# Performance work log

Measured on AMD Instinct MI355X. Metric: run time of the kernel, lower is better.

Reference implementation:

```python
import jax, jax.numpy as jnp
import numpy as np

B, T, NH, NB = 16, 400, 100, 65
SR, BLOCK = 16000, 160
REV_LEN = SR  # Reverb(sampling_rate, sampling_rate)


def _fft_convolve(signal, kernel):
    # torch: pad signal right by n, kernel left by its length, multiply spectra, keep 2nd half
    n = signal.shape[-1]
    s = jnp.pad(signal, [(0, 0)] * (signal.ndim - 1) + [(0, n)])
    k = jnp.pad(kernel, [(0, 0)] * (kernel.ndim - 1) + [(kernel.shape[-1], 0)])
    out = jnp.fft.irfft(jnp.fft.rfft(s) * jnp.fft.rfft(k), s.shape[-1])
    return out[..., out.shape[-1] // 2:]


def _amp_to_impulse_response(amp, target_size):
    # amp: [..., n_bands] real magnitudes treated as zero-phase rfft coefficients
    ir = jnp.fft.irfft(jax.lax.complex(amp, jnp.zeros_like(amp)))  # [..., 2*(NB-1)]
    fs = ir.shape[-1]
    ir = jnp.roll(ir, fs // 2, axis=-1)
    win = 0.5 - 0.5 * jnp.cos(2.0 * np.pi * jnp.arange(fs, dtype=ir.dtype) / fs)  # periodic hann
    ir = ir * win
    ir = jnp.pad(ir, [(0, 0)] * (ir.ndim - 1) + [(0, target_size - fs)])
    return jnp.roll(ir, -fs // 2, axis=-1)


def setup_inputs() -> dict:
    key = jax.random.key(0)
    ks = jax.random.split(key, 6)
    pitch = 40.0 + 400.0 * jax.random.uniform(ks[0], (B, T, 1), dtype=jnp.float32)
    total_amp = jax.random.uniform(ks[1], (B, T), dtype=jnp.float32)
    harmo_amps = jax.random.uniform(ks[2], (B, NH, T), dtype=jnp.float32) + 1e-3
    noise_filter = 0.1 * jax.random.uniform(ks[3], (B, T, NB), dtype=jnp.float32)
    noise = 2.0 * jax.random.uniform(ks[4], (B, T, BLOCK), dtype=jnp.float32) - 1.0
    reverb_noise = 2.0 * jax.random.uniform(ks[5], (REV_LEN, 1), dtype=jnp.float32) - 1.0
    decay = jnp.asarray(5.0, jnp.float32)
    wet = jnp.asarray(0.0, jnp.float32)
    return dict(pitch=pitch, total_amp=total_amp, harmo_amps=harmo_amps,
                noise_filter=noise_filter, noise=noise, reverb_noise=reverb_noise,
                decay=decay, wet=wet, sampling_rate=SR, block_size=BLOCK)


def reference(pitch, total_amp, harmo_amps, noise_filter, noise, reverb_noise,
              decay, wet, sampling_rate, block_size):
    dt = pitch.dtype
    n_harm = harmo_amps.shape[1]
    harm_idx = jnp.arange(1, n_harm + 1, dtype=dt)
    # remove_above_nyquist: mask harmonics whose freq >= sr/2 (tiny epsilon kept, as in DDSP)
    freqs = pitch[:, :, 0][:, None, :] * harm_idx[None, :, None]          # [B,NH,T]
    aa = (freqs < (sampling_rate / 2)).astype(dt) + 1e-4
    amps = harmo_amps * aa
    amps = jnp.transpose(amps, (0, 2, 1))                                  # [B,T,NH]
    amps = amps / jnp.sum(amps, axis=-1, keepdims=True)
    amps = amps * total_amp[..., None]
    # nearest-neighbor upsample by block_size (F.interpolate default mode)
    amps_up = jnp.repeat(amps, block_size, axis=1)                         # [B,N,NH]
    pitch_up = jnp.repeat(pitch, block_size, axis=1)                       # [B,N,1]
    # harmonic additive synthesis
    omega = jnp.cumsum(2.0 * np.pi * pitch_up / sampling_rate, axis=1)     # [B,N,1]
    harmonic = jnp.sum(jnp.sin(omega * harm_idx) * amps_up, axis=-1, keepdims=True)
    # filtered noise branch
    impulse = _amp_to_impulse_response(noise_filter, block_size)           # [B,T,BLOCK]
    noise_f = _fft_convolve(noise, impulse)                                # [B,T,BLOCK]
    noise_f = noise_f.reshape(noise_f.shape[0], -1, 1)                     # [B,N,1]
    signal = harmonic + noise_f
    # reverb (forward with reverb=True)
    rev_len = reverb_noise.shape[0]
    t = (jnp.arange(rev_len, dtype=dt) / sampling_rate)[None, :, None]     # [1,L,1]
    imp = reverb_noise[None] * jnp.exp(-jax.nn.softplus(-decay) * t * 500.0) * jax.nn.sigmoid(wet)
    imp = imp.at[:, 0].set(1.0)
    imp = jnp.pad(imp, ((0, 0), (0, signal.shape[1] - rev_len), (0, 0)))   # [1,N,1]
    out = _fft_convolve(signal[..., 0], imp[..., 0])[..., None]            # [B,N,1]
    return out
```

## Files before the change

kernel.cpp:

```cpp
#include <hip/hip_runtime.h>

#define B_ 16
#define T_ 400
#define NH_ 100
#define NB_ 65
#define BLK_ 160
#define SR_ 16000
#define N_ 64000
#define REV_ 16000
#define KPAD_ 16128
#define KTOT_ 80128
#define NT_ 1038
#define M_ 16
#define NWG_ 250

typedef __attribute__((ext_vector_type(8))) _Float16 f16x8;
typedef __attribute__((ext_vector_type(2))) _Float16 f16x2;
typedef __attribute__((ext_vector_type(4))) float f32x4;

static __device__ __forceinline__ float dot2f(f16x2 a, f16x2 b, float c) {
#if __has_builtin(__builtin_amdgcn_fdot2)
  return __builtin_amdgcn_fdot2(a, b, c, false);
#else
  return fmaf((float)a[0], (float)b[0], fmaf((float)a[1], (float)b[1], c));
#endif
}

__global__ __launch_bounds__(512) void k_pre(const float* __restrict__ pitch,
                                             const float* __restrict__ rn,
                                             const float* __restrict__ dec,
                                             const float* __restrict__ wet,
                                             double* __restrict__ Pv,
                                             double* __restrict__ Xv,
                                             _Float16* __restrict__ FH,
                                             _Float16* __restrict__ PH) {
  const int blk = blockIdx.x, tid = threadIdx.x;
  if (blk >= NT_) {
    __shared__ double s[512];
    const int b = blk - NT_, t = tid;
    double x = 0.0;
    if (t < T_) x = (double)pitch[b * T_ + t] * (1.0 / (double)SR_);
    s[t] = x;
    __syncthreads();
    for (int off = 1; off < 512; off <<= 1) {
      double v = (t >= off) ? s[t - off] : 0.0;
      __syncthreads();
      s[t] += v;
      __syncthreads();
    }
    if (t < T_) {
      Xv[b * T_ + t] = x;
      Pv[b * T_ + t] = (s[t] - x) * 160.0;
    }
    return;
  }
  const int t = blk;
  const int gid = t * 512 + tid;
  if (gid < 32256) ((f32x4*)PH)[gid] = (f32x4){0.f, 0.f, 0.f, 0.f};
  const int lane = tid >> 3, j = tid & 7;
  const int idx = (t - 14) * 16 + (lane & 15) - ((lane >> 4) << 3) - j;
  float v = 0.f;
  if (idx == 0) {
    v = 1.0f;
  } else if (idx > 0 && idx < REV_) {
    const float a = log1pf(expf(-dec[0]));
    const float sg = 1.f / (1.f + expf(-wet[0]));
    v = rn[idx] * expf(-a * ((float)idx / (float)SR_) * 500.0f) * sg;
  }
  FH[t * 512 + tid] = (_Float16)v;
}

__global__ __launch_bounds__(320) void k_synth(
    const float* __restrict__ pitch, const float* __restrict__ tamp,
    const float* __restrict__ harmo, const float* __restrict__ nfilt,
    const float* __restrict__ noise, const double* __restrict__ Pv,
    const double* __restrict__ Xv, _Float16* __restrict__ PH) {
  const int tid = threadIdx.x;
  const int g = (tid >= 160) ? 1 : 0;
  const int ltid = tid - (g << 7) - (g << 5);
  const int bt = (blockIdx.x << 1) + g;
  const int b = bt / T_, t = bt - b * T_;
  __shared__ __align__(16) float amp[2][112];
  __shared__ __align__(16) float a_s[2][68];
  __shared__ __align__(16) float ir_s[2][68];
  __shared__ __align__(16) _Float16 C0[2][320];
  __shared__ __align__(16) _Float16 C1[2][320];
  __shared__ __align__(16) _Float16 imp_sw[2][128];
  __shared__ float red_s[2];

  const float pv = pitch[bt];
  int nv = (int)(8000.0f / pv);
  if (nv > NH_) nv = NH_;
  while (nv < NH_ && (float)(nv + 1) * pv < 8000.0f) ++nv;
  while (nv > 0 && (float)nv * pv >= 8000.0f) --nv;

  if (ltid < NB_) a_s[g][ltid] = nfilt[bt * NB_ + ltid];
  {
    const _Float16 nh = (_Float16)noise[bt * BLK_ + ltid];
    C0[g][160 + ltid] = nh;
    C1[g][159 + ltid] = nh;
    C0[g][ltid] = (_Float16)0.f;
    if (ltid < 159) C1[g][ltid] = (_Float16)0.f;
  }
  if (ltid < NH_) {
    const float ha = harmo[(b * NH_ + ltid) * T_ + t];
    const float aa = (pv * (float)(ltid + 1) < 8000.0f ? 1.0f : 0.0f) + 1e-4f;
    amp[g][ltid] = ha * aa;
  } else if (ltid < 112) {
    amp[g][ltid] = 0.f;
  }
  __syncthreads();

  float irv = 0.f;
  if (ltid < 65) {
    const float phi = (float)ltid * (1.0f / 128.0f);
    const float c1 = __builtin_amdgcn_cosf(phi);
    const float c2 = fmaf(2.f * c1, c1, -1.f);
    const float c3 = fmaf(2.f * c2, c1, -c1);
    const float c4 = fmaf(2.f * c2, c2, -1.f);
    const float tc = 2.f * c4;
    float x0 = 1.f, p0 = c4;
    float x1 = c1, p1 = c3;
    float x2 = c2, p2 = c2;
    float x3 = c3, p3 = c1;
    float a0 = 0.f, a1 = 0.f, a2 = 0.f, a3 = 0.f;
#pragma unroll
    for (int m = 0; m < 8; ++m) {
      const f32x4 aA = *(const f32x4*)&a_s[g][m << 3];
      const f32x4 aB = *(const f32x4*)&a_s[g][(m << 3) + 4];
      a0 = fmaf(aA[0], x0, a0); const float y0 = fmaf(tc, x0, -p0);
      a1 = fmaf(aA[1], x1, a1); const float y1 = fmaf(tc, x1, -p1);
      a2 = fmaf(aA[2], x2, a2); const float y2 = fmaf(tc, x2, -p2);
      a3 = fmaf(aA[3], x3, a3); const float y3 = fmaf(tc, x3, -p3);
      a0 = fmaf(aB[0], y0, a0); const float z0 = fmaf(tc, y0, -x0); p0 = y0; x0 = z0;
      a1 = fmaf(aB[1], y1, a1); const float z1 = fmaf(tc, y1, -x1); p1 = y1; x1 = z1;
      a2 = fmaf(aB[2], y2, a2); const float z2 = fmaf(tc, y2, -x2); p2 = y2; x2 = z2;
      a3 = fmaf(aB[3], y3, a3); const float z3 = fmaf(tc, y3, -x3); p3 = y3; x3 = z3;
    }
    const float accS = (a0 + a1) + (a2 + a3);
    irv = (2.f * accS - a_s[g][0] + ((ltid & 1) ? -a_s[g][64] : a_s[g][64])) * (1.0f / 128.0f);
    ir_s[g][ltid] = irv;
  } else if (ltid >= 128) {
    const int l = ltid - 128;
    float v = amp[g][l] + amp[g][l + 32] + amp[g][l + 64] + (l < 4 ? amp[g][l + 96] : 0.f);
    v += __shfl_xor(v, 16);
    v += __shfl_xor(v, 8);
    v += __shfl_xor(v, 4);
    v += __shfl_xor(v, 2);
    v += __shfl_xor(v, 1);
    if (l == 0) red_s[g] = v;
  }
  __syncthreads();

  if (ltid < 64) {
    const float w = 0.5f + 0.5f * __builtin_amdgcn_cosf((float)ltid * (1.0f / 128.0f));
    imp_sw[g][ltid ^ 1] = (_Float16)(w * irv);
  } else if (ltid >= 96 && ltid < 160) {
    const int u = ltid - 96;
    const float w = 0.5f - 0.5f * __builtin_amdgcn_cosf((float)u * (1.0f / 128.0f));
    imp_sw[g][64 + (u ^ 1)] = (_Float16)(w * ir_s[g][64 - u]);
  }
  const float scale = tamp[bt] / red_s[g];
  double th = Pv[bt] + (double)(ltid + 1) * Xv[bt];
  th -= floor(th);
  const float theta = (float)th;
  const float cT = __builtin_amdgcn_cosf(theta);
  const float sT = __builtin_amdgcn_sinf(theta);
  __syncthreads();

  float acc;
  {
    const float c2 = fmaf(cT, cT, -sT * sT);
    const float s2 = 2.f * cT * sT;
    const float s3 = fmaf(s2, cT, c2 * sT);
    const float s4 = 2.f * s2 * c2;
    const float c4 = fmaf(2.f * c2, c2, -1.f);
    const float tc = 2.f * c4;
    float x0 = sT, p0 = -s3;
    float x1 = s2, p1 = -s2;
    float x2 = s3, p2 = -sT;
    float x3 = s4, p3 = 0.f;
    float a0 = 0.f, a1 = 0.f, a2 = 0.f, a3 = 0.f;
    const int S = (nv + 7) >> 3;
    for (int m = 0; m < S; ++m) {
      const f32x4 aA = *(const f32x4*)&amp[g][m << 3];
      const f32x4 aB = *(const f32x4*)&amp[g][(m << 3) + 4];
      a0 = fmaf(aA[0], x0, a0); const float y0 = fmaf(tc, x0, -p0);
      a1 = fmaf(aA[1], x1, a1); const float y1 = fmaf(tc, x1, -p1);
      a2 = fmaf(aA[2], x2, a2); const float y2 = fmaf(tc, x2, -p2);
      a3 = fmaf(aA[3], x3, a3); const float y3 = fmaf(tc, x3, -p3);
      a0 = fmaf(aB[0], y0, a0); const float z0 = fmaf(tc, y0, -x0); p0 = y0; x0 = z0;
      a1 = fmaf(aB[1], y1, a1); const float z1 = fmaf(tc, y1, -x1); p1 = y1; x1 = z1;
      a2 = fmaf(aB[2], y2, a2); const float z2 = fmaf(tc, y2, -x2); p2 = y2; x2 = z2;
      a3 = fmaf(aB[3], y3, a3); const float z3 = fmaf(tc, y3, -x3); p3 = y3; x3 = z3;
    }
    acc = ((a0 + a1) + (a2 + a3)) * scale;
  }

  float nf = 0.f;
  {
    const f16x2* np0;
    int pe;
    if (ltid & 1) {
      np0 = (const f16x2*)C0[g];
      pe = (159 + ltid) >> 1;
    } else {
      np0 = (const f16x2*)C1[g];
      pe = (158 + ltid) >> 1;
    }
    const f16x8* ip = (const f16x8*)imp_sw[g];
#pragma unroll
    for (int k0 = 0; k0 < 8; ++k0) {
      const f16x8 i8 = ip[k0];
      const int kb = k0 << 2;
      nf = dot2f((f16x2){i8[0], i8[1]}, np0[pe - kb], nf);
      nf = dot2f((f16x2){i8[2], i8[3]}, np0[pe - kb - 1], nf);
      nf = dot2f((f16x2){i8[4], i8[5]}, np0[pe - kb - 2], nf);
      nf = dot2f((f16x2){i8[6], i8[7]}, np0[pe - kb - 3], nf);
    }
#pragma unroll
    for (int k0 = 0; k0 < 8; ++k0) {
      const f16x8 i8 = ip[8 + k0];
      const int kb = (k0 << 2) + 48;
      nf = dot2f((f16x2){i8[0], i8[1]}, np0[pe - kb], nf);
      nf = dot2f((f16x2){i8[2], i8[3]}, np0[pe - kb - 1], nf);
      nf = dot2f((f16x2){i8[4], i8[5]}, np0[pe - kb - 2], nf);
      nf = dot2f((f16x2){i8[6], i8[7]}, np0[pe - kb - 3], nf);
    }
  }

  const float v = acc + nf;
  const unsigned k = (unsigned)(KPAD_ + t * BLK_ + ltid);
  const unsigned off = ((k >> 3) << 7) + ((unsigned)b << 3) + (k & 7u);
  PH[off] = (_Float16)v;
}

static __device__ __forceinline__ f32x4 mfma_f16(f16x8 a, f16x8 b, f32x4 c) {
  return __builtin_amdgcn_mfma_f32_16x16x32_f16(a, b, c, 0, 0, 0);
}

template <int U, bool ISSUE, bool CONSUME>
__device__ __forceinline__ void conv_step(f16x8 (&Rh)[M_], f32x4 (&acc)[M_], f16x8& bhi,
                                          f16x8 (&nb)[2], f16x8 (&na0)[2], f16x8 (&na1)[2],
                                          const f16x8* __restrict__ ph,
                                          const f16x8* __restrict__ fh,
                                          int& kit, int& tit) {
  if (ISSUE) {
    kit += 64;
    nb[U & 1] = ph[kit];
    tit -= 2;
    na0[U & 1] = fh[tit * 64];
    na1[U & 1] = fh[(tit + 1) * 64];
  }
#pragma unroll
  for (int m = 0; m < M_; ++m) {
    const int sl = (m - 2 * U) & (M_ - 1);
    acc[m] = mfma_f16(Rh[sl], bhi, acc[m]);
  }
  if (CONSUME) {
    Rh[(M_ - 2 - 2 * U) & (M_ - 1)] = na0[(U + 1) & 1];
    Rh[(M_ - 1 - 2 * U) & (M_ - 1)] = na1[(U + 1) & 1];
    bhi = nb[(U + 1) & 1];
  }
}

__global__ __launch_bounds__(512) void k_mconv(const f16x8* __restrict__ FH,
                                               const f16x8* __restrict__ PH,
                                               float* __restrict__ out) {
  const int tid = threadIdx.x;
  const int s = tid >> 6, lane = tid & 63;
  int w = blockIdx.x;
  {
    const int q = NWG_ / 8, r = NWG_ % 8;
    const int xcd = w & 7, o = w >> 3;
    w = (xcd < r ? xcd * (q + 1) : r * (q + 1) + (xcd - r) * q) + o;
  }
  const int Q0 = w << 8;
  const int T0 = 1022 - 128 * s;

  const f16x8* fh = FH + lane;
  f16x8 Rh[M_];
#pragma unroll
  for (int m = 0; m < M_; ++m) Rh[m] = fh[(T0 + m) * 64];
  f32x4 acc[M_];
#pragma unroll
  for (int m = 0; m < M_; ++m) acc[m] = (f32x4){0.f, 0.f, 0.f, 0.f};

  const f16x8* ph = PH + ((lane >> 4) << 4) + (lane & 15);
  int kit = (Q0 + 2048 * s) << 1;
  int tit = T0;
  f16x8 bhi = ph[kit];
  f16x8 nb[2], na0[2], na1[2];
  kit += 64;
  nb[1] = ph[kit];
  tit -= 2;
  na0[1] = fh[tit * 64];
  na1[1] = fh[(tit + 1) * 64];

  for (int ii = 0; ii < 7; ++ii) {
    conv_step<0, true, true>(Rh, acc, bhi, nb, na0, na1, ph, fh, kit, tit);
    conv_step<1, true, true>(Rh, acc, bhi, nb, na0, na1, ph, fh, kit, tit);
    conv_step<2, true, true>(Rh, acc, bhi, nb, na0, na1, ph, fh, kit, tit);
    conv_step<3, true, true>(Rh, acc, bhi, nb, na0, na1, ph, fh, kit, tit);
    conv_step<4, true, true>(Rh, acc, bhi, nb, na0, na1, ph, fh, kit, tit);
    conv_step<5, true, true>(Rh, acc, bhi, nb, na0, na1, ph, fh, kit, tit);
    conv_step<6, true, true>(Rh, acc, bhi, nb, na0, na1, ph, fh, kit, tit);
    conv_step<7, true, true>(Rh, acc, bhi, nb, na0, na1, ph, fh, kit, tit);
  }
  conv_step<0, true, true>(Rh, acc, bhi, nb, na0, na1, ph, fh, kit, tit);
  conv_step<1, true, true>(Rh, acc, bhi, nb, na0, na1, ph, fh, kit, tit);
  conv_step<2, true, true>(Rh, acc, bhi, nb, na0, na1, ph, fh, kit, tit);
  conv_step<3, true, true>(Rh, acc, bhi, nb, na0, na1, ph, fh, kit, tit);
  conv_step<4, true, true>(Rh, acc, bhi, nb, na0, na1, ph, fh, kit, tit);
  conv_step<5, true, true>(Rh, acc, bhi, nb, na0, na1, ph, fh, kit, tit);
  conv_step<6, false, true>(Rh, acc, bhi, nb, na0, na1, ph, fh, kit, tit);
  conv_step<7, false, false>(Rh, acc, bhi, nb, na0, na1, ph, fh, kit, tit);

  __shared__ f32x4 part[4][M_][64];
  if (s < 4) {
#pragma unroll
    for (int m = 0; m < M_; ++m) part[s][m][lane] = acc[m];
  }
  __syncthreads();
  if (s >= 4) {
#pragma unroll
    for (int m = 0; m < M_; ++m) part[s - 4][m][lane] += acc[m];
  }
  __syncthreads();
#pragma unroll
  for (int half = 0; half < 2; ++half) {
    const int it = tid + (half << 9);
    const int m = it >> 6, ln = it & 63;
    f32x4 v = part[0][m][ln];
    v += part[1][m][ln];
    v += part[2][m][ln];
    v += part[3][m][ln];
    const int b = ln & 15, gq = ln >> 4;
    *(f32x4*)(out + (size_t)b * N_ + Q0 + (m << 4) + (gq << 2)) = v;
  }
}

extern "C" void kernel_launch(void* const* d_in, const int* in_sizes, int n_in,
                              void* d_out, int out_size, void* d_ws, size_t ws_size,
                              hipStream_t stream) {
  const float* pitch = (const float*)d_in[0];
  const float* tamp  = (const float*)d_in[1];
  const float* harmo = (const float*)d_in[2];
  const float* nfilt = (const float*)d_in[3];
  const float* noise = (const float*)d_in[4];
  const float* rn    = (const float*)d_in[5];
  const float* dec   = (const float*)d_in[6];
  const float* wet   = (const float*)d_in[7];

  char* ws = (char*)d_ws;
  size_t off = 0;
  _Float16* PH = (_Float16*)(ws + off); off += (size_t)KTOT_ * 16 * 2;
  _Float16* FH = (_Float16*)(ws + off); off += (size_t)NT_ * 512 * 2;
  double* Pv = (double*)(ws + off);     off += (size_t)B_ * T_ * 8;
  double* Xv = (double*)(ws + off);     off += (size_t)B_ * T_ * 8;
  float* out = (float*)d_out;

  k_pre<<<dim3(NT_ + B_), dim3(512), 0, stream>>>(pitch, rn, dec, wet, Pv, Xv, FH, PH);
  k_synth<<<dim3(B_ * T_ / 2), dim3(320), 0, stream>>>(pitch, tamp, harmo, nfilt, noise, Pv, Xv, PH);
  k_mconv<<<dim3(NWG_), dim3(512), 0, stream>>>((const f16x8*)FH, (const f16x8*)PH, out);
}
```

Baseline: 60.83 us.

## Replace pre-expanded Toeplitz fragment table with compact reversed impulse arrays

The reverb impulse is no longer expanded into a large per-tile Toeplitz fragment table (about 1 MB of f16). Instead k_pre writes two reversed copies of the impulse, one per parity offset, and the convolution kernel builds each MFMA A fragment with unaligned 4-byte loads from them. The goal is to shrink k_pre's work and the footprint the conv kernel reads, so fragments stay in cache. The MFMA loop also double-buffers the B operand and rotates the accumulator issue order to ease dependency stalls. The cost is four 32-bit loads per fragment instead of one 128-bit load.

```diff
diff --git a/kernel.cpp b/kernel.cpp
--- a/kernel.cpp
+++ b/kernel.cpp
@@ -10,9 +10,9 @@
 #define REV_ 16000
 #define KPAD_ 16128
 #define KTOT_ 80128
-#define NT_ 1038
 #define M_ 16
 #define NWG_ 250
+#define ISTRIDE_ 16768
 
 typedef __attribute__((ext_vector_type(8))) _Float16 f16x8;
 typedef __attribute__((ext_vector_type(2))) _Float16 f16x2;
@@ -32,42 +32,47 @@
                                              const float* __restrict__ wet,
                                              double* __restrict__ Pv,
                                              double* __restrict__ Xv,
-                                             _Float16* __restrict__ FH,
+                                             _Float16* __restrict__ IMPREV,
                                              _Float16* __restrict__ PH) {
   const int blk = blockIdx.x, tid = threadIdx.x;
-  if (blk >= NT_) {
-    __shared__ double s[512];
-    const int b = blk - NT_, t = tid;
-    double x = 0.0;
-    if (t < T_) x = (double)pitch[b * T_ + t] * (1.0 / (double)SR_);
-    s[t] = x;
+  if (blk < 66) {
+    const int gid = blk * 512 + tid;
+    if (gid < 2 * ISTRIDE_) {
+      const int c = gid / ISTRIDE_, u = gid - c * ISTRIDE_;
+      const int i = 16383 - u - c;
+      float v = 0.f;
+      if (i == 0) {
+        v = 1.0f;
+      } else if (i > 0 && i < REV_) {
+        const float a = log1pf(expf(-dec[0]));
+        const float sg = 1.f / (1.f + expf(-wet[0]));
+        v = rn[i] * expf(-a * ((float)i / (float)SR_) * 500.0f) * sg;
+      }
+      IMPREV[gid] = (_Float16)v;
+    }
+    return;
+  }
+  if (blk < 129) {
+    const int gid = (blk - 66) * 512 + tid;
+    ((f32x4*)PH)[gid] = (f32x4){0.f, 0.f, 0.f, 0.f};
+    return;
+  }
+  __shared__ double s[512];
+  const int b = blk - 129, t = tid;
+  double x = 0.0;
+  if (t < T_) x = (double)pitch[b * T_ + t] * (1.0 / (double)SR_);
+  s[t] = x;
+  __syncthreads();
+  for (int off = 1; off < 512; off <<= 1) {
+    double v = (t >= off) ? s[t - off] : 0.0;
     __syncthreads();
-    for (int off = 1; off < 512; off <<= 1) {
-      double v = (t >= off) ? s[t - off] : 0.0;
-      __syncthreads();
-      s[t] += v;
-      __syncthreads();
-    }
-    if (t < T_) {
-      Xv[b * T_ + t] = x;
-      Pv[b * T_ + t] = (s[t] - x) * 160.0;
-    }
-    return;
-  }
-  const int t = blk;
-  const int gid = t * 512 + tid;
-  if (gid < 32256) ((f32x4*)PH)[gid] = (f32x4){0.f, 0.f, 0.f, 0.f};
-  const int lane = tid >> 3, j = tid & 7;
-  const int idx = (t - 14) * 16 + (lane & 15) - ((lane >> 4) << 3) - j;
-  float v = 0.f;
-  if (idx == 0) {
-    v = 1.0f;
-  } else if (idx > 0 && idx < REV_) {
-    const float a = log1pf(expf(-dec[0]));
-    const float sg = 1.f / (1.f + expf(-wet[0]));
-    v = rn[idx] * expf(-a * ((float)idx / (float)SR_) * 500.0f) * sg;
-  }
-  FH[t * 512 + tid] = (_Float16)v;
+    s[t] += v;
+    __syncthreads();
+  }
+  if (t < T_) {
+    Xv[b * T_ + t] = x;
+    Pv[b * T_ + t] = (s[t] - x) * 160.0;
+  }
 }
 
 __global__ __launch_bounds__(320) void k_synth(
@@ -239,32 +244,40 @@
   return __builtin_amdgcn_mfma_f32_16x16x32_f16(a, b, c, 0, 0, 0);
 }
 
+static __device__ __forceinline__ f16x8 lfrag(const unsigned short* __restrict__ base, int byteoff) {
+  const unsigned* p = (const unsigned*)((const char*)base + byteoff);
+  union { unsigned u[4]; f16x8 v; } x;
+  x.u[0] = p[0]; x.u[1] = p[1]; x.u[2] = p[2]; x.u[3] = p[3];
+  return x.v;
+}
+
 template <int U, bool ISSUE, bool CONSUME>
-__device__ __forceinline__ void conv_step(f16x8 (&Rh)[M_], f32x4 (&acc)[M_], f16x8& bhi,
+__device__ __forceinline__ void conv_step(f16x8 (&Rh)[M_], f32x4 (&acc)[M_], f16x8 (&bhi2)[2],
                                           f16x8 (&nb)[2], f16x8 (&na0)[2], f16x8 (&na1)[2],
                                           const f16x8* __restrict__ ph,
-                                          const f16x8* __restrict__ fh,
-                                          int& kit, int& tit) {
+                                          const unsigned short* __restrict__ abase,
+                                          int& kit, int& abyte) {
   if (ISSUE) {
     kit += 64;
     nb[U & 1] = ph[kit];
-    tit -= 2;
-    na0[U & 1] = fh[tit * 64];
-    na1[U & 1] = fh[(tit + 1) * 64];
-  }
-#pragma unroll
-  for (int m = 0; m < M_; ++m) {
+    abyte += 64;
+    na0[U & 1] = lfrag(abase, abyte);
+    na1[U & 1] = lfrag(abase, abyte - 32);
+  }
+#pragma unroll
+  for (int mm = 0; mm < M_; ++mm) {
+    const int m = (mm + M_ - 2) & (M_ - 1);
     const int sl = (m - 2 * U) & (M_ - 1);
-    acc[m] = mfma_f16(Rh[sl], bhi, acc[m]);
+    acc[m] = mfma_f16(Rh[sl], bhi2[U & 1], acc[m]);
   }
   if (CONSUME) {
     Rh[(M_ - 2 - 2 * U) & (M_ - 1)] = na0[(U + 1) & 1];
     Rh[(M_ - 1 - 2 * U) & (M_ - 1)] = na1[(U + 1) & 1];
-    bhi = nb[(U + 1) & 1];
-  }
-}
-
-__global__ __launch_bounds__(512) void k_mconv(const f16x8* __restrict__ FH,
+    bhi2[(U + 1) & 1] = nb[(U + 1) & 1];
+  }
+}
+
+__global__ __launch_bounds__(512) void k_mconv(const unsigned short* __restrict__ IMPREV,
                                                const f16x8* __restrict__ PH,
                                                float* __restrict__ out) {
   const int tid = threadIdx.x;
@@ -278,43 +291,47 @@
   const int Q0 = w << 8;
   const int T0 = 1022 - 128 * s;
 
-  const f16x8* fh = FH + lane;
+  const int pat = (lane & 15) - ((lane >> 4) << 3);
+  const int o0 = 16223 - 16 * T0 - pat;
+  const int par = o0 & 1;
+  const unsigned short* abase = IMPREV + (par ? ISTRIDE_ : 0);
+  int abyte = 2 * (384 + o0 - par);
+
   f16x8 Rh[M_];
 #pragma unroll
-  for (int m = 0; m < M_; ++m) Rh[m] = fh[(T0 + m) * 64];
+  for (int m = 0; m < M_; ++m) Rh[m] = lfrag(abase, abyte - 32 * m);
   f32x4 acc[M_];
 #pragma unroll
   for (int m = 0; m < M_; ++m) acc[m] = (f32x4){0.f, 0.f, 0.f, 0.f};
 
   const f16x8* ph = PH + ((lane >> 4) << 4) + (lane & 15);
   int kit = (Q0 + 2048 * s) << 1;
-  int tit = T0;
-  f16x8 bhi = ph[kit];
-  f16x8 nb[2], na0[2], na1[2];
+  f16x8 bhi2[2], nb[2], na0[2], na1[2];
+  bhi2[0] = ph[kit];
   kit += 64;
   nb[1] = ph[kit];
-  tit -= 2;
-  na0[1] = fh[tit * 64];
-  na1[1] = fh[(tit + 1) * 64];
+  abyte += 64;
+  na0[1] = lfrag(abase, abyte);
+  na1[1] = lfrag(abase, abyte - 32);
 
   for (int ii = 0; ii < 7; ++ii) {
-    conv_step<0, true, true>(Rh, acc, bhi, nb, na0, na1, ph, fh, kit, tit);
-    conv_step<1, true, true>(Rh, acc, bhi, nb, na0, na1, ph, fh, kit, tit);
-    conv_step<2, true, true>(Rh, acc, bhi, nb, na0, na1, ph, fh, kit, tit);
-    conv_step<3, true, true>(Rh, acc, bhi, nb, na0, na1, ph, fh, kit, tit);
-    conv_step<4, true, true>(Rh, acc, bhi, nb, na0, na1, ph, fh, kit, tit);
-    conv_step<5, true, true>(Rh, acc, bhi, nb, na0, na1, ph, fh, kit, tit);
-    conv_step<6, true, true>(Rh, acc, bhi, nb, na0, na1, ph, fh, kit, tit);
-    conv_step<7, true, true>(Rh, acc, bhi, nb, na0, na1, ph, fh, kit, tit);
-  }
-  conv_step<0, true, true>(Rh, acc, bhi, nb, na0, na1, ph, fh, kit, tit);
-  conv_step<1, true, true>(Rh, acc, bhi, nb, na0, na1, ph, fh, kit, tit);
-  conv_step<2, true, true>(Rh, acc, bhi, nb, na0, na1, ph, fh, kit, tit);
-  conv_step<3, true, true>(Rh, acc, bhi, nb, na0, na1, ph, fh, kit, tit);
-  conv_step<4, true, true>(Rh, acc, bhi, nb, na0, na1, ph, fh, kit, tit);
-  conv_step<5, true, true>(Rh, acc, bhi, nb, na0, na1, ph, fh, kit, tit);
-  conv_step<6, false, true>(Rh, acc, bhi, nb, na0, na1, ph, fh, kit, tit);
-  conv_step<7, false, false>(Rh, acc, bhi, nb, na0, na1, ph, fh, kit, tit);
+    conv_step<0, true, true>(Rh, acc, bhi2, nb, na0, na1, ph, abase, kit, abyte);
+    conv_step<1, true, true>(Rh, acc, bhi2, nb, na0, na1, ph, abase, kit, abyte);
+    conv_step<2, true, true>(Rh, acc, bhi2, nb, na0, na1, ph, abase, kit, abyte);
+    conv_step<3, true, true>(Rh, acc, bhi2, nb, na0, na1, ph, abase, kit, abyte);
+    conv_step<4, true, true>(Rh, acc, bhi2, nb, na0, na1, ph, abase, kit, abyte);
+    conv_step<5, true, true>(Rh, acc, bhi2, nb, na0, na1, ph, abase, kit, abyte);
+    conv_step<6, true, true>(Rh, acc, bhi2, nb, na0, na1, ph, abase, kit, abyte);
+    conv_step<7, true, true>(Rh, acc, bhi2, nb, na0, na1, ph, abase, kit, abyte);
+  }
+  conv_step<0, true, true>(Rh, acc, bhi2, nb, na0, na1, ph, abase, kit, abyte);
+  conv_step<1, true, true>(Rh, acc, bhi2, nb, na0, na1, ph, abase, kit, abyte);
+  conv_step<2, true, true>(Rh, acc, bhi2, nb, na0, na1, ph, abase, kit, abyte);
+  conv_step<3, true, true>(Rh, acc, bhi2, nb, na0, na1, ph, abase, kit, abyte);
+  conv_step<4, true, true>(Rh, acc, bhi2, nb, na0, na1, ph, abase, kit, abyte);
+  conv_step<5, true, true>(Rh, acc, bhi2, nb, na0, na1, ph, abase, kit, abyte);
+  conv_step<6, false, true>(Rh, acc, bhi2, nb, na0, na1, ph, abase, kit, abyte);
+  conv_step<7, false, false>(Rh, acc, bhi2, nb, na0, na1, ph, abase, kit, abyte);
 
   __shared__ f32x4 part[4][M_][64];
   if (s < 4) {
@@ -354,13 +371,13 @@
 
   char* ws = (char*)d_ws;
   size_t off = 0;
-  _Float16* PH = (_Float16*)(ws + off); off += (size_t)KTOT_ * 16 * 2;
-  _Float16* FH = (_Float16*)(ws + off); off += (size_t)NT_ * 512 * 2;
-  double* Pv = (double*)(ws + off);     off += (size_t)B_ * T_ * 8;
-  double* Xv = (double*)(ws + off);     off += (size_t)B_ * T_ * 8;
+  _Float16* PH = (_Float16*)(ws + off);     off += (size_t)KTOT_ * 16 * 2;
+  _Float16* IMPREV = (_Float16*)(ws + off); off += (size_t)2 * ISTRIDE_ * 2;
+  double* Pv = (double*)(ws + off);         off += (size_t)B_ * T_ * 8;
+  double* Xv = (double*)(ws + off);         off += (size_t)B_ * T_ * 8;
   float* out = (float*)d_out;
 
-  k_pre<<<dim3(NT_ + B_), dim3(512), 0, stream>>>(pitch, rn, dec, wet, Pv, Xv, FH, PH);
+  k_pre<<<dim3(145), dim3(512), 0, stream>>>(pitch, rn, dec, wet, Pv, Xv, IMPREV, PH);
   k_synth<<<dim3(B_ * T_ / 2), dim3(320), 0, stream>>>(pitch, tamp, harmo, nfilt, noise, Pv, Xv, PH);
-  k_mconv<<<dim3(NWG_), dim3(512), 0, stream>>>((const f16x8*)FH, (const f16x8*)PH, out);
-}
+  k_mconv<<<dim3(NWG_), dim3(512), 0, stream>>>((const unsigned short*)IMPREV, (const f16x8*)PH, out);
+}
```

Result: faster. 58.89 us (-3.2%).
